# Kernel tuning notes

Hardware: AMD Instinct MI355X
Metric: run time of the kernel (lower is better)

## Reference

```python
import jax, jax.numpy as jnp
import numpy as np

N_NODES = 50000
N_EDGES = 800000
IN_DIM = 128
HID = 8
HEADS = 8
OUT_DIM = 64
NEG_SLOPE = 0.2


def setup_inputs() -> dict:
    key = jax.random.key(0)
    ks = jax.random.split(key, 8)
    x = jax.random.normal(ks[0], (N_NODES, IN_DIM), dtype=jnp.float32)
    edge_index = jax.random.randint(ks[1], (2, N_EDGES), 0, N_NODES, dtype=jnp.int64)
    W1 = jax.random.normal(ks[2], (IN_DIM, HEADS * HID), dtype=jnp.float32) / np.sqrt(IN_DIM)
    a_src1 = jax.random.normal(ks[3], (HEADS, HID), dtype=jnp.float32)
    a_dst1 = jax.random.normal(ks[4], (HEADS, HID), dtype=jnp.float32)
    b1 = jnp.zeros((HEADS * HID,), dtype=jnp.float32)
    W2 = jax.random.normal(ks[5], (HEADS * HID, OUT_DIM), dtype=jnp.float32) / np.sqrt(HEADS * HID)
    a_src2 = jax.random.normal(ks[6], (1, OUT_DIM), dtype=jnp.float32)
    a_dst2 = jax.random.normal(ks[7], (1, OUT_DIM), dtype=jnp.float32)
    b2 = jnp.zeros((OUT_DIM,), dtype=jnp.float32)
    return {"x": x, "edge_index": edge_index, "W1": W1, "a_src1": a_src1,
            "a_dst1": a_dst1, "b1": b1, "W2": W2, "a_src2": a_src2,
            "a_dst2": a_dst2, "b2": b2}


def gat_conv(x, src, dst, W, a_src, a_dst, b, heads, ch):
    # PyG GATConv (eval mode): linear -> per-edge LeakyReLU score ->
    # segment-softmax over incoming edges -> weighted scatter-add -> +bias
    n = x.shape[0]
    h = (x @ W).reshape(n, heads, ch)               # [N,H,C]
    score_src = jnp.einsum('nhc,hc->nh', h, a_src)  # [N,H]
    score_dst = jnp.einsum('nhc,hc->nh', h, a_dst)  # [N,H]
    e = jax.nn.leaky_relu(score_src[src] + score_dst[dst], NEG_SLOPE)  # [E,H]
    m = jax.ops.segment_max(e, dst, num_segments=n)
    m = jnp.where(jnp.isfinite(m), m, 0.0)
    p = jnp.exp(e - m[dst])
    denom = jax.ops.segment_sum(p, dst, num_segments=n)
    alpha = p / (denom[dst] + 1e-16)                # [E,H]
    out = jax.ops.segment_sum(h[src] * alpha[:, :, None], dst, num_segments=n)
    return out.reshape(n, heads * ch) + b


def reference(x, edge_index, W1, a_src1, a_dst1, b1, W2, a_src2, a_dst2, b2):
    n = x.shape[0]
    # add_self_loops=True (PyG default)
    loops = jnp.arange(n, dtype=edge_index.dtype)
    src = jnp.concatenate([edge_index[0], loops])
    dst = jnp.concatenate([edge_index[1], loops])
    h = gat_conv(x, src, dst, W1, a_src1, a_dst1, b1, HEADS, HID)
    h = jax.nn.elu(h)
    out = gat_conv(h, src, dst, W2, a_src2, a_dst2, b2, 1, OUT_DIM)
    return out
```

## Files before the change

kernel.cpp:

```cpp
#include <hip/hip_runtime.h>
#include <hip/hip_fp16.h>
#include <math.h>
#include <stdint.h>

#define N_NODES 50000
#define N_EDGES 800000
#define ET (N_EDGES + N_NODES)
#define IN_DIM 128
#define H1DIM 64
#define HEADS 8
#define HID 8
#define OUT_DIM 64
#define NEG_SLOPE 0.2f

#define NB ((N_NODES + 255) / 256)
#define CAP 5120
#define RC2 4

#define LIN1_WAVES (N_NODES / 16)
#define LIN1_BLOCKS ((LIN1_WAVES + 3) / 4)

#define EPT 4
#define HB ((N_EDGES + 256*EPT - 1) / (256*EPT))

typedef _Float16 half8 __attribute__((ext_vector_type(8)));
typedef float f32x4 __attribute__((ext_vector_type(4)));

__device__ __forceinline__ float lrelu(float v) { return v >= 0.f ? v : NEG_SLOPE * v; }

__device__ __forceinline__ void fma8raw(uint4 u, float alpha, float* a) {
    float2 f0 = __half22float2(*(const __half2*)&u.x);
    float2 f1 = __half22float2(*(const __half2*)&u.y);
    float2 f2 = __half22float2(*(const __half2*)&u.z);
    float2 f3 = __half22float2(*(const __half2*)&u.w);
    a[0] += f0.x * alpha; a[1] += f0.y * alpha;
    a[2] += f1.x * alpha; a[3] += f1.y * alpha;
    a[4] += f2.x * alpha; a[5] += f2.y * alpha;
    a[6] += f3.x * alpha; a[7] += f3.y * alpha;
}

__device__ __forceinline__ void fma8h(const __half* __restrict__ base, float alpha, float* a) {
    fma8raw(*reinterpret_cast<const uint4*>(base), alpha, a);
}


__global__ __launch_bounds__(256) void prep_kernel(
    const float* __restrict__ W1, const float* __restrict__ W2,
    __half* __restrict__ w1fH, __half* __restrict__ w1fL,
    __half* __restrict__ w2fH, __half* __restrict__ w2fL,
    int* __restrict__ cursor)
{
    int b = blockIdx.x;
    if (b < 32) {
        int idx = b * 256 + threadIdx.x;
        int f = idx >> 9, rr = idx & 511;
        int l = rr >> 3, j = rr & 7;
        int ks = f >> 2, ct = f & 3;
        int k = ks * 32 + ((l >> 4) << 3) + j;
        int c = (ct << 4) + (l & 15);
        float w = W1[k * 64 + c];
        __half hi = __float2half(w);
        w1fH[idx] = hi;
        w1fL[idx] = __float2half(w - __half2float(hi));
    } else if (b < 48) {
        int idx = (b - 32) * 256 + threadIdx.x;
        int f = idx >> 9, rr = idx & 511;
        int l = rr >> 3, j = rr & 7;
        int ks = f >> 2, ct = f & 3;
        int k = ks * 32 + ((l >> 4) << 3) + j;
        int c = (ct << 4) + (l & 15);
        float w = W2[k * 64 + c];
        __half hi = __float2half(w);
        w2fH[idx] = hi;
        w2fL[idx] = __float2half(w - __half2float(hi));
    } else {
        for (int k = threadIdx.x; k < 16 * NB; k += 256) cursor[k] = 0;
    }
}


__global__ __launch_bounds__(256) void cl1_kernel(
    const int* __restrict__ ei, int* __restrict__ cursor, int* __restrict__ ebuf,
    const float* __restrict__ x,
    const __half* __restrict__ w1fH, const __half* __restrict__ w1fL,
    const float* __restrict__ a_src, const float* __restrict__ a_dst,
    __half* __restrict__ h1, float* __restrict__ ssrc, float* __restrict__ sdst)
{
    __shared__ int hist[NB];
    __shared__ int res[NB];
    if (blockIdx.x < HB) {
        for (int k = threadIdx.x; k < NB; k += 256) hist[k] = 0;
        __syncthreads();
        int base = blockIdx.x * (256 * EPT) + threadIdx.x;
        int ss[EPT], ds[EPT];
        #pragma unroll
        for (int j = 0; j < EPT; ++j) {
            int e = base + j * 256;
            ds[j] = -1;
            if (e < N_EDGES) {
                ss[j] = ei[e];
                ds[j] = ei[N_EDGES + e];
                atomicAdd(&hist[ds[j] >> 8], 1);
            }
        }
        __syncthreads();
        if (threadIdx.x < NB) {
            int h = hist[threadIdx.x];
            res[threadIdx.x] = h ? atomicAdd(&cursor[threadIdx.x * 16], h) : 0;
            hist[threadIdx.x] = 0;
        }
        __syncthreads();
        #pragma unroll
        for (int j = 0; j < EPT; ++j) {
            if (ds[j] >= 0) {
                int b = ds[j] >> 8;
                int r = atomicAdd(&hist[b], 1);
                int idx = res[b] + r;
                if (idx < CAP) ebuf[b * CAP + idx] = ss[j] | ((ds[j] & 255) << 16);
            }
        }
        return;
    }

    int wid = threadIdx.x >> 6, t = threadIdx.x & 63;
    int g = (blockIdx.x - HB) * 4 + wid;
    if (g >= LIN1_WAVES) return;
    int n0 = g * 16;
    int row = t & 15, kq = t >> 4;

    f32x4 acc[4] = {};
    const float* xp = x + (size_t)(n0 + row) * IN_DIM + kq * 8;
    #pragma unroll
    for (int ks = 0; ks < 4; ++ks) {
        float4 u0 = *reinterpret_cast<const float4*>(xp + ks * 32);
        float4 u1 = *reinterpret_cast<const float4*>(xp + ks * 32 + 4);
        float xv[8] = {u0.x, u0.y, u0.z, u0.w, u1.x, u1.y, u1.z, u1.w};
        half8 ah, al;
        #pragma unroll
        for (int j = 0; j < 8; ++j) {
            _Float16 h = (_Float16)xv[j];
            ah[j] = h;
            al[j] = (_Float16)(xv[j] - (float)h);
        }
        #pragma unroll
        for (int ct = 0; ct < 4; ++ct) {
            int f = ks * 4 + ct;
            half8 bh = *reinterpret_cast<const half8*>(w1fH + f * 512 + t * 8);
            half8 bl = *reinterpret_cast<const half8*>(w1fL + f * 512 + t * 8);
            acc[ct] = __builtin_amdgcn_mfma_f32_16x16x32_f16(ah, bh, acc[ct], 0, 0, 0);
            acc[ct] = __builtin_amdgcn_mfma_f32_16x16x32_f16(al, bh, acc[ct], 0, 0, 0);
            acc[ct] = __builtin_amdgcn_mfma_f32_16x16x32_f16(ah, bl, acc[ct], 0, 0, 0);
        }
    }

    float asv[4], adv[4];
    #pragma unroll
    for (int ct = 0; ct < 4; ++ct) {
        asv[ct] = a_src[ct * 16 + (t & 15)];
        adv[ct] = a_dst[ct * 16 + (t & 15)];
    }
    int rbase = n0 + (t >> 4) * 4;
    #pragma unroll
    for (int r = 0; r < 4; ++r) {
        int n = rbase + r;
        #pragma unroll
        for (int ct = 0; ct < 4; ++ct) {
            float v = acc[ct][r];
            h1[(size_t)n * 64 + ct * 16 + (t & 15)] = __float2half(v);
            float ps = v * asv[ct], pd = v * adv[ct];
            ps += __shfl_xor(ps, 1); ps += __shfl_xor(ps, 2); ps += __shfl_xor(ps, 4);
            pd += __shfl_xor(pd, 1); pd += __shfl_xor(pd, 2); pd += __shfl_xor(pd, 4);
            if ((t & 7) == 0) {
                int hd = ct * 2 + ((t >> 3) & 1);
                ssrc[n * 8 + hd] = ps;
                sdst[n * 8 + hd] = pd;
            }
        }
    }
}


__global__ __launch_bounds__(256) void bscan_kernel(
    const int* __restrict__ cursor, int* __restrict__ ebase, int* __restrict__ rowp)
{
    __shared__ int sh[256];
    int t = threadIdx.x;
    int cnt = (t < NB) ? cursor[t * 16] : 0;
    sh[t] = cnt;
    __syncthreads();
    #pragma unroll
    for (int off = 1; off < 256; off <<= 1) {
        int add = (t >= off) ? sh[t - off] : 0;
        __syncthreads();
        sh[t] += add;
        __syncthreads();
    }
    if (t < NB) ebase[t] = sh[t] - cnt;
    if (t == 0) rowp[N_NODES] = ET;
}


__global__ __launch_bounds__(256) void p2_kernel(
    const int* __restrict__ ebase, const int* __restrict__ cursor,
    const int* __restrict__ ebuf, int* __restrict__ rowp, int* __restrict__ adj)
{
    __shared__ int cnt[256];
    __shared__ int sh[256];
    __shared__ int cur[256];
    int b = blockIdx.x, t = threadIdx.x;
    int n0 = b * 256;
    int nn = N_NODES - n0; if (nn > 256) nn = 256;
    cnt[t] = (t < nn) ? 1 : 0;
    __syncthreads();
    int m = cursor[b * 16];
    const int* eb = ebuf + b * CAP;
    for (int e = t; e < m; e += 256)
        atomicAdd(&cnt[eb[e] >> 16], 1);
    __syncthreads();
    int myc = cnt[t];
    sh[t] = myc;
    __syncthreads();
    #pragma unroll
    for (int o = 1; o < 256; o <<= 1) {
        int add = (t >= o) ? sh[t - o] : 0;
        __syncthreads();
        sh[t] += add;
        __syncthreads();
    }
    int ab = ebase[b] + n0;
    int myoff = ab + sh[t] - myc;
    cur[t] = myoff;
    if (t < nn) rowp[n0 + t] = myoff;
    __syncthreads();
    for (int e = t; e < m; e += 256) {
        int v = eb[e];
        int r = atomicAdd(&cur[v >> 16], 1);
        adj[r] = v & 0xFFFF;
    }
    if (t < nn) adj[myoff + myc - 1] = n0 + t;
}


__global__ __launch_bounds__(256) void l1_kernel(
    const int* __restrict__ row, const int* __restrict__ adj,
    const __half* __restrict__ h1, const float* __restrict__ s1, const float* __restrict__ t1,
    const float* __restrict__ b1, __half* __restrict__ ha)
{
    int wid = threadIdx.x >> 6, t = threadIdx.x & 63;
    int n = blockIdx.x * 4 + wid;
    int beg = row[n], end = row[n + 1];
    int slot = t >> 3, h = t & 7;
    float sd = t1[n * 8 + h];
    const int e0 = beg + slot;

    int   sv[RC2];
    float p[RC2];
    uint4 raw[RC2];
    float m = -3e38f;
    #pragma unroll
    for (int it = 0; it < RC2; ++it) {
        int e = e0 + it * 8;
        bool ok = e < end;
        int s = ok ? adj[e] : n;
        sv[it] = s;
        float v = ok ? lrelu(s1[s * 8 + h] + sd) : -3e38f;
        p[it] = v;
        m = fmaxf(m, v);
        raw[it] = *reinterpret_cast<const uint4*>(h1 + (size_t)s * 64 + h * 8);
    }
    for (int e = e0 + RC2 * 8; e < end; e += 8)
        m = fmaxf(m, lrelu(s1[adj[e] * 8 + h] + sd));
    m = fmaxf(m, __shfl_xor(m, 8));
    m = fmaxf(m, __shfl_xor(m, 16));
    m = fmaxf(m, __shfl_xor(m, 32));

    float den = 0.f;
    #pragma unroll
    for (int it = 0; it < RC2; ++it) {
        float pe = __expf(p[it] - m);
        p[it] = pe;
        den += pe;
    }
    for (int e = e0 + RC2 * 8; e < end; e += 8)
        den += __expf(lrelu(s1[adj[e] * 8 + h] + sd) - m);
    den += __shfl_xor(den, 8);
    den += __shfl_xor(den, 16);
    den += __shfl_xor(den, 32);
    float inv = 1.f / (den + 1e-16f);

    float a[8] = {0,0,0,0,0,0,0,0};
    #pragma unroll
    for (int it = 0; it < RC2; ++it) fma8raw(raw[it], p[it] * inv, a);
    for (int e = e0 + RC2 * 8; e < end; e += 8) {
        int s = adj[e];
        float alpha = __expf(lrelu(s1[s * 8 + h] + sd) - m) * inv;
        fma8h(h1 + (size_t)s * 64 + h * 8, alpha, a);
    }
    #pragma unroll
    for (int j = 0; j < 8; ++j) {
        a[j] += __shfl_xor(a[j], 8);
        a[j] += __shfl_xor(a[j], 16);
        a[j] += __shfl_xor(a[j], 32);
    }

    if (slot < 4) {
        int j0 = slot * 2;
        float v0 = a[j0]     + b1[h * 8 + j0];
        float v1 = a[j0 + 1] + b1[h * 8 + j0 + 1];
        v0 = v0 > 0.f ? v0 : (__expf(v0) - 1.f);
        v1 = v1 > 0.f ? v1 : (__expf(v1) - 1.f);
        __half2 hv;
        hv.x = __float2half(v0);
        hv.y = __float2half(v1);
        *reinterpret_cast<__half2*>(ha + (size_t)n * 64 + h * 8 + j0) = hv;
    }
}


__global__ __launch_bounds__(256) void lin2_kernel(
    const __half* __restrict__ ha,
    const __half* __restrict__ w2fH, const __half* __restrict__ w2fL,
    const float* __restrict__ as2, const float* __restrict__ ad2,
    __half* __restrict__ h2, float* __restrict__ s2, float* __restrict__ t2)
{
    int tid = threadIdx.x;
    int wid = tid >> 6, t = tid & 63;
    int g = blockIdx.x * 4 + wid;
    if (g >= LIN1_WAVES) return;
    int n0 = g * 16;
    int row = t & 15, kq = t >> 4;

    f32x4 acc[4] = {};
    const __half* xp = ha + (size_t)(n0 + row) * 64 + kq * 8;
    #pragma unroll
    for (int ks = 0; ks < 2; ++ks) {
        half8 ahv = *reinterpret_cast<const half8*>(xp + ks * 32);
        #pragma unroll
        for (int ct = 0; ct < 4; ++ct) {
            int f = ks * 4 + ct;
            half8 bh = *reinterpret_cast<const half8*>(w2fH + f * 512 + t * 8);
            half8 bl = *reinterpret_cast<const half8*>(w2fL + f * 512 + t * 8);
            acc[ct] = __builtin_amdgcn_mfma_f32_16x16x32_f16(ahv, bh, acc[ct], 0, 0, 0);
            acc[ct] = __builtin_amdgcn_mfma_f32_16x16x32_f16(ahv, bl, acc[ct], 0, 0, 0);
        }
    }

    float asv[4], adv[4];
    #pragma unroll
    for (int ct = 0; ct < 4; ++ct) {
        asv[ct] = as2[ct * 16 + (t & 15)];
        adv[ct] = ad2[ct * 16 + (t & 15)];
    }
    int rbase = n0 + (t >> 4) * 4;
    #pragma unroll
    for (int r = 0; r < 4; ++r) {
        int n = rbase + r;
        float ps = 0.f, pd = 0.f;
        #pragma unroll
        for (int ct = 0; ct < 4; ++ct) {
            float v = acc[ct][r];
            h2[(size_t)n * 64 + ct * 16 + (t & 15)] = __float2half(v);
            ps += v * asv[ct];
            pd += v * adv[ct];
        }
        ps += __shfl_xor(ps, 1); ps += __shfl_xor(ps, 2);
        ps += __shfl_xor(ps, 4); ps += __shfl_xor(ps, 8);
        pd += __shfl_xor(pd, 1); pd += __shfl_xor(pd, 2);
        pd += __shfl_xor(pd, 4); pd += __shfl_xor(pd, 8);
        if ((t & 15) == 0) { s2[n] = ps; t2[n] = pd; }
    }
}


__global__ __launch_bounds__(256) void l2_kernel(
    const int* __restrict__ row, const int* __restrict__ adj,
    const __half* __restrict__ h2, const float* __restrict__ s2, const float* __restrict__ t2,
    const float* __restrict__ b2, float* __restrict__ out)
{
    int wid = threadIdx.x >> 6, t = threadIdx.x & 63;
    int n = blockIdx.x * 4 + wid;
    int beg = row[n], end = row[n + 1];
    int slot = t >> 3, g = t & 7;
    float sd = t2[n];
    const int e0 = beg + slot;

    int   sv[RC2];
    float p[RC2];
    uint4 raw[RC2];
    float m = -3e38f;
    #pragma unroll
    for (int it = 0; it < RC2; ++it) {
        int e = e0 + it * 8;
        bool ok = e < end;
        int s = ok ? adj[e] : n;
        sv[it] = s;
        float v = ok ? lrelu(s2[s] + sd) : -3e38f;
        p[it] = v;
        m = fmaxf(m, v);
        raw[it] = *reinterpret_cast<const uint4*>(h2 + (size_t)s * 64 + g * 8);
    }
    for (int e = e0 + RC2 * 8; e < end; e += 8)
        m = fmaxf(m, lrelu(s2[adj[e]] + sd));
    m = fmaxf(m, __shfl_xor(m, 8));
    m = fmaxf(m, __shfl_xor(m, 16));
    m = fmaxf(m, __shfl_xor(m, 32));

    float den = 0.f;
    #pragma unroll
    for (int it = 0; it < RC2; ++it) {
        float pe = __expf(p[it] - m);
        p[it] = pe;
        den += pe;
    }
    for (int e = e0 + RC2 * 8; e < end; e += 8)
        den += __expf(lrelu(s2[adj[e]] + sd) - m);
    den += __shfl_xor(den, 8);
    den += __shfl_xor(den, 16);
    den += __shfl_xor(den, 32);
    float inv = 1.f / (den + 1e-16f);

    float a[8] = {0,0,0,0,0,0,0,0};
    #pragma unroll
    for (int it = 0; it < RC2; ++it) fma8raw(raw[it], p[it] * inv, a);
    for (int e = e0 + RC2 * 8; e < end; e += 8) {
        int s = adj[e];
        float alpha = __expf(lrelu(s2[s] + sd) - m) * inv;
        fma8h(h2 + (size_t)s * 64 + g * 8, alpha, a);
    }
    #pragma unroll
    for (int j = 0; j < 8; ++j) {
        a[j] += __shfl_xor(a[j], 8);
        a[j] += __shfl_xor(a[j], 16);
        a[j] += __shfl_xor(a[j], 32);
    }
    if (slot == 0) {
        float4 o0 = make_float4(a[0] + b2[g * 8 + 0], a[1] + b2[g * 8 + 1],
                                a[2] + b2[g * 8 + 2], a[3] + b2[g * 8 + 3]);
        float4 o1 = make_float4(a[4] + b2[g * 8 + 4], a[5] + b2[g * 8 + 5],
                                a[6] + b2[g * 8 + 6], a[7] + b2[g * 8 + 7]);
        float4* op = (float4*)(out + (size_t)n * 64 + g * 8);
        op[0] = o0; op[1] = o1;
    }
}

extern "C" void kernel_launch(void* const* d_in, const int* in_sizes, int n_in,
                              void* d_out, int out_size, void* d_ws, size_t ws_size,
                              hipStream_t stream)
{
    const float* x   = (const float*)d_in[0];
    const int* ei    = (const int*)d_in[1];
    const float* W1  = (const float*)d_in[2];
    const float* as1 = (const float*)d_in[3];
    const float* ad1 = (const float*)d_in[4];
    const float* b1  = (const float*)d_in[5];
    const float* W2  = (const float*)d_in[6];
    const float* as2 = (const float*)d_in[7];
    const float* ad2 = (const float*)d_in[8];
    const float* b2  = (const float*)d_in[9];
    float* out = (float*)d_out;

    char* wsb = (char*)d_ws;
    __half* h1   = (__half*)wsb;
    __half* h2   = h1 + (size_t)N_NODES * 64;
    __half* ha   = h2 + (size_t)N_NODES * 64;
    __half* w1fH = ha + (size_t)N_NODES * 64;
    __half* w1fL = w1fH + 8192;
    __half* w2fH = w1fL + 8192;
    __half* w2fL = w2fH + 4096;
    float*  s1   = (float*)(w2fL + 4096);
    float*  t1   = s1 + N_NODES * 8;
    float*  s2   = t1 + N_NODES * 8;
    float*  t2   = s2 + N_NODES;
    int*    cursor = (int*)(t2 + N_NODES);
    int*    ebase  = cursor + 16 * NB;
    int*    rowp   = ebase + NB + 1;
    int*    adj    = rowp + N_NODES + 1;
    int*    ebuf   = adj + ET;

    prep_kernel<<<49, 256, 0, stream>>>(W1, W2, w1fH, w1fL, w2fH, w2fL, cursor);

    cl1_kernel<<<HB + LIN1_BLOCKS, 256, 0, stream>>>(ei, cursor, ebuf, x, w1fH, w1fL,
                                                     as1, ad1, h1, s1, t1);

    bscan_kernel<<<1, 256, 0, stream>>>(cursor, ebase, rowp);
    p2_kernel<<<NB, 256, 0, stream>>>(ebase, cursor, ebuf, rowp, adj);

    l1_kernel<<<N_NODES / 4, 256, 0, stream>>>(rowp, adj, h1, s1, t1, b1, ha);

    lin2_kernel<<<LIN1_BLOCKS, 256, 0, stream>>>(ha, w2fH, w2fL, as2, ad2, h2, s2, t2);

    l2_kernel<<<N_NODES / 4, 256, 0, stream>>>(rowp, adj, h2, s2, t2, b2, out);
}
```

Measured before the change: 199.2 us.

## Fuse block scan into p2 and layer-1 aggregation with lin2 via shared memory

Drops the separate single-block scan kernel by having every p2 block redundantly compute the prefix sum over per-bucket counts. It also fuses the layer-1 neighbour aggregation with the second linear MFMA projection: 16 waves per 1024-thread block write ELU outputs into shared memory, and wave 0 then runs the MFMA and score reduction. This removes two kernel launches and the global round trip of the ha intermediate. In exchange, the 1024-thread blocks may lower occupancy, and 15 of the 16 waves sit idle during the MFMA phase.

```diff
diff --git a/kernel.cpp b/kernel.cpp
--- a/kernel.cpp
+++ b/kernel.cpp
@@ -180,39 +180,33 @@
 }
 
 
-__global__ __launch_bounds__(256) void bscan_kernel(
-    const int* __restrict__ cursor, int* __restrict__ ebase, int* __restrict__ rowp)
-{
-    __shared__ int sh[256];
-    int t = threadIdx.x;
-    int cnt = (t < NB) ? cursor[t * 16] : 0;
-    sh[t] = cnt;
-    __syncthreads();
-    #pragma unroll
-    for (int off = 1; off < 256; off <<= 1) {
-        int add = (t >= off) ? sh[t - off] : 0;
-        __syncthreads();
-        sh[t] += add;
-        __syncthreads();
-    }
-    if (t < NB) ebase[t] = sh[t] - cnt;
-    if (t == 0) rowp[N_NODES] = ET;
-}
-
-
 __global__ __launch_bounds__(256) void p2_kernel(
-    const int* __restrict__ ebase, const int* __restrict__ cursor,
-    const int* __restrict__ ebuf, int* __restrict__ rowp, int* __restrict__ adj)
-{
+    const int* __restrict__ cursor, const int* __restrict__ ebuf,
+    int* __restrict__ rowp, int* __restrict__ adj)
+{
+    __shared__ int sb[256];
     __shared__ int cnt[256];
     __shared__ int sh[256];
     __shared__ int cur[256];
     int b = blockIdx.x, t = threadIdx.x;
+
+    int bc = (t < NB) ? cursor[t * 16] : 0;
+    sb[t] = bc;
+    __syncthreads();
+    #pragma unroll
+    for (int o = 1; o < 256; o <<= 1) {
+        int add = (t >= o) ? sb[t - o] : 0;
+        __syncthreads();
+        sb[t] += add;
+        __syncthreads();
+    }
+    int m = cursor[b * 16];
+    int eb0 = sb[b] - m;
+
     int n0 = b * 256;
     int nn = N_NODES - n0; if (nn > 256) nn = 256;
     cnt[t] = (t < nn) ? 1 : 0;
     __syncthreads();
-    int m = cursor[b * 16];
     const int* eb = ebuf + b * CAP;
     for (int e = t; e < m; e += 256)
         atomicAdd(&cnt[eb[e] >> 16], 1);
@@ -227,10 +221,11 @@
         sh[t] += add;
         __syncthreads();
     }
-    int ab = ebase[b] + n0;
+    int ab = eb0 + n0;
     int myoff = ab + sh[t] - myc;
     cur[t] = myoff;
     if (t < nn) rowp[n0 + t] = myoff;
+    if (b == 0 && t == 0) rowp[N_NODES] = ET;
     __syncthreads();
     for (int e = t; e < m; e += 256) {
         int v = eb[e];
@@ -241,19 +236,23 @@
 }
 
 
-__global__ __launch_bounds__(256) void l1_kernel(
+__global__ __launch_bounds__(1024) void l1f_kernel(
     const int* __restrict__ row, const int* __restrict__ adj,
     const __half* __restrict__ h1, const float* __restrict__ s1, const float* __restrict__ t1,
-    const float* __restrict__ b1, __half* __restrict__ ha)
-{
+    const float* __restrict__ b1,
+    const __half* __restrict__ w2fH, const __half* __restrict__ w2fL,
+    const float* __restrict__ as2, const float* __restrict__ ad2,
+    __half* __restrict__ h2, float* __restrict__ s2, float* __restrict__ t2)
+{
+    __shared__ __half haS[16 * 64];
     int wid = threadIdx.x >> 6, t = threadIdx.x & 63;
-    int n = blockIdx.x * 4 + wid;
+    int n0b = blockIdx.x * 16;
+    int n = n0b + wid;
     int beg = row[n], end = row[n + 1];
     int slot = t >> 3, h = t & 7;
     float sd = t1[n * 8 + h];
     const int e0 = beg + slot;
 
-    int   sv[RC2];
     float p[RC2];
     uint4 raw[RC2];
     float m = -3e38f;
@@ -262,7 +261,6 @@
         int e = e0 + it * 8;
         bool ok = e < end;
         int s = ok ? adj[e] : n;
-        sv[it] = s;
         float v = ok ? lrelu(s1[s * 8 + h] + sd) : -3e38f;
         p[it] = v;
         m = fmaxf(m, v);
@@ -312,26 +310,14 @@
         __half2 hv;
         hv.x = __float2half(v0);
         hv.y = __float2half(v1);
-        *reinterpret_cast<__half2*>(ha + (size_t)n * 64 + h * 8 + j0) = hv;
-    }
-}
-
-
-__global__ __launch_bounds__(256) void lin2_kernel(
-    const __half* __restrict__ ha,
-    const __half* __restrict__ w2fH, const __half* __restrict__ w2fL,
-    const float* __restrict__ as2, const float* __restrict__ ad2,
-    __half* __restrict__ h2, float* __restrict__ s2, float* __restrict__ t2)
-{
-    int tid = threadIdx.x;
-    int wid = tid >> 6, t = tid & 63;
-    int g = blockIdx.x * 4 + wid;
-    if (g >= LIN1_WAVES) return;
-    int n0 = g * 16;
-    int row = t & 15, kq = t >> 4;
-
+        *reinterpret_cast<__half2*>(&haS[wid * 64 + h * 8 + j0]) = hv;
+    }
+    __syncthreads();
+
+    if (wid != 0) return;
+    int rowi = t & 15, kq = t >> 4;
     f32x4 acc[4] = {};
-    const __half* xp = ha + (size_t)(n0 + row) * 64 + kq * 8;
+    const __half* xp = haS + rowi * 64 + kq * 8;
     #pragma unroll
     for (int ks = 0; ks < 2; ++ks) {
         half8 ahv = *reinterpret_cast<const half8*>(xp + ks * 32);
@@ -351,15 +337,15 @@
         asv[ct] = as2[ct * 16 + (t & 15)];
         adv[ct] = ad2[ct * 16 + (t & 15)];
     }
-    int rbase = n0 + (t >> 4) * 4;
+    int rbase = n0b + (t >> 4) * 4;
     #pragma unroll
     for (int r = 0; r < 4; ++r) {
-        int n = rbase + r;
+        int nn2 = rbase + r;
         float ps = 0.f, pd = 0.f;
         #pragma unroll
         for (int ct = 0; ct < 4; ++ct) {
             float v = acc[ct][r];
-            h2[(size_t)n * 64 + ct * 16 + (t & 15)] = __float2half(v);
+            h2[(size_t)nn2 * 64 + ct * 16 + (t & 15)] = __float2half(v);
             ps += v * asv[ct];
             pd += v * adv[ct];
         }
@@ -367,7 +353,7 @@
         ps += __shfl_xor(ps, 4); ps += __shfl_xor(ps, 8);
         pd += __shfl_xor(pd, 1); pd += __shfl_xor(pd, 2);
         pd += __shfl_xor(pd, 4); pd += __shfl_xor(pd, 8);
-        if ((t & 15) == 0) { s2[n] = ps; t2[n] = pd; }
+        if ((t & 15) == 0) { s2[nn2] = ps; t2[nn2] = pd; }
     }
 }
 
@@ -384,7 +370,6 @@
     float sd = t2[n];
     const int e0 = beg + slot;
 
-    int   sv[RC2];
     float p[RC2];
     uint4 raw[RC2];
     float m = -3e38f;
@@ -393,7 +378,6 @@
         int e = e0 + it * 8;
         bool ok = e < end;
         int s = ok ? adj[e] : n;
-        sv[it] = s;
         float v = ok ? lrelu(s2[s] + sd) : -3e38f;
         p[it] = v;
         m = fmaxf(m, v);
@@ -462,8 +446,7 @@
     char* wsb = (char*)d_ws;
     __half* h1   = (__half*)wsb;
     __half* h2   = h1 + (size_t)N_NODES * 64;
-    __half* ha   = h2 + (size_t)N_NODES * 64;
-    __half* w1fH = ha + (size_t)N_NODES * 64;
+    __half* w1fH = h2 + (size_t)N_NODES * 64;
     __half* w1fL = w1fH + 8192;
     __half* w2fH = w1fL + 8192;
     __half* w2fL = w2fH + 4096;
@@ -472,8 +455,7 @@
     float*  s2   = t1 + N_NODES * 8;
     float*  t2   = s2 + N_NODES;
     int*    cursor = (int*)(t2 + N_NODES);
-    int*    ebase  = cursor + 16 * NB;
-    int*    rowp   = ebase + NB + 1;
+    int*    rowp   = cursor + 16 * NB;
     int*    adj    = rowp + N_NODES + 1;
     int*    ebuf   = adj + ET;
 
@@ -482,12 +464,10 @@
     cl1_kernel<<<HB + LIN1_BLOCKS, 256, 0, stream>>>(ei, cursor, ebuf, x, w1fH, w1fL,
                                                      as1, ad1, h1, s1, t1);
 
-    bscan_kernel<<<1, 256, 0, stream>>>(cursor, ebase, rowp);
-    p2_kernel<<<NB, 256, 0, stream>>>(ebase, cursor, ebuf, rowp, adj);
-
-    l1_kernel<<<N_NODES / 4, 256, 0, stream>>>(rowp, adj, h1, s1, t1, b1, ha);
-
-    lin2_kernel<<<LIN1_BLOCKS, 256, 0, stream>>>(ha, w2fH, w2fL, as2, ad2, h2, s2, t2);
+    p2_kernel<<<NB, 256, 0, stream>>>(cursor, ebuf, rowp, adj);
+
+    l1f_kernel<<<N_NODES / 16, 1024, 0, stream>>>(rowp, adj, h1, s1, t1, b1,
+                                                  w2fH, w2fL, as2, ad2, h2, s2, t2);
 
     l2_kernel<<<N_NODES / 4, 256, 0, stream>>>(rowp, adj, h2, s2, t2, b2, out);
 }
```

New measurement: 216.0 us. 8.4% more time.

## Fold block-offset scan into CSR build kernel and widen it to 512 threads

Applied to the files above, without the earlier changes.

The single-block bscan kernel is removed. Each p2 block now redundantly computes the prefix sum over per-bucket counts itself, and the kernel runs 512 threads per block for the scatter loops. The self-loop adjacency write moves to a separate small p2b kernel, and edges-per-thread in the edge-bucketing pass doubles from 4 to 8. This trades one serial launch for redundant per-block scans plus an extra tiny launch, and the larger EPT means fewer edge-bucketing blocks.

```diff
diff --git a/kernel.cpp b/kernel.cpp
--- a/kernel.cpp
+++ b/kernel.cpp
@@ -20,7 +20,7 @@
 #define LIN1_WAVES (N_NODES / 16)
 #define LIN1_BLOCKS ((LIN1_WAVES + 3) / 4)
 
-#define EPT 4
+#define EPT 8
 #define HB ((N_EDGES + 256*EPT - 1) / (256*EPT))
 
 typedef _Float16 half8 __attribute__((ext_vector_type(8)));
@@ -180,64 +180,66 @@
 }
 
 
-__global__ __launch_bounds__(256) void bscan_kernel(
-    const int* __restrict__ cursor, int* __restrict__ ebase, int* __restrict__ rowp)
-{
-    __shared__ int sh[256];
-    int t = threadIdx.x;
-    int cnt = (t < NB) ? cursor[t * 16] : 0;
-    sh[t] = cnt;
-    __syncthreads();
-    #pragma unroll
-    for (int off = 1; off < 256; off <<= 1) {
-        int add = (t >= off) ? sh[t - off] : 0;
-        __syncthreads();
-        sh[t] += add;
-        __syncthreads();
-    }
-    if (t < NB) ebase[t] = sh[t] - cnt;
-    if (t == 0) rowp[N_NODES] = ET;
-}
-
-
-__global__ __launch_bounds__(256) void p2_kernel(
-    const int* __restrict__ ebase, const int* __restrict__ cursor,
-    const int* __restrict__ ebuf, int* __restrict__ rowp, int* __restrict__ adj)
-{
+__global__ __launch_bounds__(512) void p2_kernel(
+    const int* __restrict__ cursor, const int* __restrict__ ebuf,
+    int* __restrict__ rowp, int* __restrict__ adj)
+{
+    __shared__ int sb[256];
     __shared__ int cnt[256];
     __shared__ int sh[256];
     __shared__ int cur[256];
     int b = blockIdx.x, t = threadIdx.x;
+
+    if (t < 256) sb[t] = (t < NB) ? cursor[t * 16] : 0;
+    __syncthreads();
+    #pragma unroll
+    for (int o = 1; o < 256; o <<= 1) {
+        int add = (t < 256 && t >= o) ? sb[t - o] : 0;
+        __syncthreads();
+        if (t < 256) sb[t] += add;
+        __syncthreads();
+    }
+    int m = cursor[b * 16];
+    int eb0 = sb[b] - m;
+
     int n0 = b * 256;
     int nn = N_NODES - n0; if (nn > 256) nn = 256;
-    cnt[t] = (t < nn) ? 1 : 0;
+    if (t < 256) cnt[t] = (t < nn) ? 1 : 0;
     __syncthreads();
-    int m = cursor[b * 16];
     const int* eb = ebuf + b * CAP;
-    for (int e = t; e < m; e += 256)
+    for (int e = t; e < m; e += 512)
         atomicAdd(&cnt[eb[e] >> 16], 1);
     __syncthreads();
-    int myc = cnt[t];
-    sh[t] = myc;
+    int myc = (t < 256) ? cnt[t] : 0;
+    if (t < 256) sh[t] = myc;
     __syncthreads();
     #pragma unroll
     for (int o = 1; o < 256; o <<= 1) {
-        int add = (t >= o) ? sh[t - o] : 0;
-        __syncthreads();
-        sh[t] += add;
-        __syncthreads();
-    }
-    int ab = ebase[b] + n0;
-    int myoff = ab + sh[t] - myc;
-    cur[t] = myoff;
-    if (t < nn) rowp[n0 + t] = myoff;
+        int add = (t < 256 && t >= o) ? sh[t - o] : 0;
+        __syncthreads();
+        if (t < 256) sh[t] += add;
+        __syncthreads();
+    }
+    int ab = eb0 + n0;
+    if (t < 256) {
+        int myoff = ab + sh[t] - myc;
+        cur[t] = myoff;
+        if (t < nn) rowp[n0 + t] = myoff;
+        if (b == 0 && t == 0) rowp[N_NODES] = ET;
+    }
     __syncthreads();
-    for (int e = t; e < m; e += 256) {
+    for (int e = t; e < m; e += 512) {
         int v = eb[e];
         int r = atomicAdd(&cur[v >> 16], 1);
         adj[r] = v & 0xFFFF;
     }
-    if (t < nn) adj[myoff + myc - 1] = n0 + t;
+}
+
+__global__ __launch_bounds__(256) void p2b_kernel(
+    const int* __restrict__ rowp, int* __restrict__ adj)
+{
+    int n = blockIdx.x * 256 + threadIdx.x;
+    if (n < N_NODES) adj[rowp[n + 1] - 1] = n;
 }
 
 
@@ -253,7 +255,6 @@
     float sd = t1[n * 8 + h];
     const int e0 = beg + slot;
 
-    int   sv[RC2];
     float p[RC2];
     uint4 raw[RC2];
     float m = -3e38f;
@@ -262,7 +263,6 @@
         int e = e0 + it * 8;
         bool ok = e < end;
         int s = ok ? adj[e] : n;
-        sv[it] = s;
         float v = ok ? lrelu(s1[s * 8 + h] + sd) : -3e38f;
         p[it] = v;
         m = fmaxf(m, v);
@@ -384,7 +384,6 @@
     float sd = t2[n];
     const int e0 = beg + slot;
 
-    int   sv[RC2];
     float p[RC2];
     uint4 raw[RC2];
     float m = -3e38f;
@@ -393,7 +392,6 @@
         int e = e0 + it * 8;
         bool ok = e < end;
         int s = ok ? adj[e] : n;
-        sv[it] = s;
         float v = ok ? lrelu(s2[s] + sd) : -3e38f;
         p[it] = v;
         m = fmaxf(m, v);
@@ -472,8 +470,7 @@
     float*  s2   = t1 + N_NODES * 8;
     float*  t2   = s2 + N_NODES;
     int*    cursor = (int*)(t2 + N_NODES);
-    int*    ebase  = cursor + 16 * NB;
-    int*    rowp   = ebase + NB + 1;
+    int*    rowp   = cursor + 16 * NB;
     int*    adj    = rowp + N_NODES + 1;
     int*    ebuf   = adj + ET;
 
@@ -482,8 +479,8 @@
     cl1_kernel<<<HB + LIN1_BLOCKS, 256, 0, stream>>>(ei, cursor, ebuf, x, w1fH, w1fL,
                                                      as1, ad1, h1, s1, t1);
 
-    bscan_kernel<<<1, 256, 0, stream>>>(cursor, ebase, rowp);
-    p2_kernel<<<NB, 256, 0, stream>>>(ebase, cursor, ebuf, rowp, adj);
+    p2_kernel<<<NB, 512, 0, stream>>>(cursor, ebuf, rowp, adj);
+    p2b_kernel<<<(N_NODES + 255) / 256, 256, 0, stream>>>(rowp, adj);
 
     l1_kernel<<<N_NODES / 4, 256, 0, stream>>>(rowp, adj, h1, s1, t1, b1, ha);
 
```

Measured after the change: 190.0 us. -4.6%, faster.
